# Kernel tuning notes

Measured on AMD Instinct MI355X. Metric: run time of the kernel, lower is better.

## Reference

```python
import jax, jax.numpy as jnp
import numpy as np

TEMPERATURE_F = 0.5  # init kwarg temperature_f
B = 4096
D = 256


def setup_inputs() -> dict:
    key = jax.random.key(0)
    k1, k2 = jax.random.split(key)
    h_i = jax.random.normal(k1, (B, D), dtype=jnp.float32)
    h_j = jax.random.normal(k2, (B, D), dtype=jnp.float32)
    return {"h_i": h_i, "h_j": h_j, "batch_size": B}


def reference(h_i, h_j, batch_size):
    # NT-Xent / InfoNCE (forward_feature_InfoNCE).
    # Original: logits = [pos | sim[neg_mask].reshape(N,-1)], labels = 0,
    # CrossEntropyLoss(reduction='sum') / N.
    # The logit set per row i is {positive} U {negatives} = all sim[i, :] except
    # the diagonal (self) entry, since neg_mask removes diagonal + positive pair
    # and the positive is prepended back. So CE reduces to logsumexp over the
    # off-diagonal row minus the positive logit.
    N = 2 * batch_size
    h = jnp.concatenate([h_i, h_j], axis=0)                    # [N, D]
    sim = jnp.matmul(h, h.T) / TEMPERATURE_F                   # [N, N]
    pos = jnp.concatenate([
        jnp.diagonal(sim, offset=batch_size),                  # sim_i_j
        jnp.diagonal(sim, offset=-batch_size),                 # sim_j_i
    ])                                                         # [N]
    denom_mask = ~jnp.eye(N, dtype=bool)                       # drop self-sim only
    neg_inf = jnp.finfo(sim.dtype).min
    lse = jax.nn.logsumexp(jnp.where(denom_mask, sim, neg_inf), axis=1)  # [N]
    loss = jnp.sum(lse - pos) / N
    return loss
```

## Files before the change

### kernel.cpp

```cpp
#include <hip/hip_runtime.h>
#include <stdint.h>

#define N_TOT 8192
#define DIM   256
#define BHALF 4096
#define BM    256
#define CT    64
#define NC    16
#define CW    (N_TOT / NC)
#define NTILE (CW / CT)

#define SCALEF 2.8853900817779268f
#define LN2F   0.69314718055994531f
#define SHIFT2 200.0f

typedef __attribute__((ext_vector_type(8))) short bf16x8;
typedef __attribute__((ext_vector_type(4))) float f32x4;

typedef const __attribute__((address_space(1))) void* gas_ptr;
typedef __attribute__((address_space(3))) void* lds_ptr;

#if __has_builtin(__builtin_amdgcn_exp2f)
__device__ inline float exp2v(float x) { return __builtin_amdgcn_exp2f(x); }
#else
__device__ inline float exp2v(float x) { return exp2f(x); }
#endif

__device__ inline float bf2f(ushort u) { return __uint_as_float(((uint32_t)u) << 16); }

__device__ inline ushort f2bf(float f) {
  uint32_t u = __float_as_uint(f);
  u = (u + 0x7fffu + ((u >> 16) & 1u)) >> 16;
  return (ushort)u;
}

__global__ void conv_kernel(const float* __restrict__ hi, const float* __restrict__ hj,
                            ushort* __restrict__ hb) {
  int t = blockIdx.x * blockDim.x + threadIdx.x;
  const int half4 = BHALF * DIM / 4;
  float4 v = (t < half4) ? ((const float4*)hi)[t] : ((const float4*)hj)[t - half4];
  ushort4 o;
  o.x = f2bf(v.x); o.y = f2bf(v.y); o.z = f2bf(v.z); o.w = f2bf(v.w);
  ((ushort4*)hb)[t] = o;
}

__global__ void pos_kernel(const ushort* __restrict__ hb, float* __restrict__ pos2) {
  int gw = (blockIdx.x * blockDim.x + threadIdx.x) >> 6;
  int l = threadIdx.x & 63;
  if (gw >= N_TOT) return;
  int j = (gw < BHALF) ? gw + BHALF : gw - BHALF;
  const ushort4* a = (const ushort4*)(hb + (size_t)gw * DIM);
  const ushort4* b = (const ushort4*)(hb + (size_t)j * DIM);
  ushort4 av = a[l], bv = b[l];
  float acc = bf2f(av.x) * bf2f(bv.x) + bf2f(av.y) * bf2f(bv.y)
            + bf2f(av.z) * bf2f(bv.z) + bf2f(av.w) * bf2f(bv.w);
  #pragma unroll
  for (int d = 1; d < 64; d <<= 1) acc += __shfl_xor(acc, d, 64);
  if (l == 0) pos2[gw] = acc * SCALEF;
}

__global__ __launch_bounds__(256, 1)
void lse_stage1(const ushort* __restrict__ hb, float* __restrict__ wsum) {
  const int tid = threadIdx.x;
  const int w  = tid >> 6;
  const int l  = tid & 63;
  const int lg = l >> 4;
  const int ll = l & 15;
  const int row0  = blockIdx.x * BM + w * 64;
  const int cbase = blockIdx.y * CW;

  __shared__ ushort Bt[2][CT * DIM];

  bf16x8 afrag[4][8];
  #pragma unroll
  for (int r = 0; r < 4; ++r) {
    const ushort* ap = hb + (size_t)(row0 + r * 16 + ll) * DIM + lg * 8;
    #pragma unroll
    for (int q = 0; q < 8; ++q) afrag[r][q] = *(const bf16x8*)(ap + q * 32);
  }

  float s[16];
  #pragma unroll
  for (int i = 0; i < 16; ++i) s[i] = 0.0f;
  const float NEGINF = -__builtin_inff();

  auto stage = [&](int buf, int t) {
    const int c0 = cbase + t * CT;
    #pragma unroll
    for (int q = 0; q < 8; ++q) {
      int a    = w * 8192 + q * 1024 + l * 16;
      int trow = a >> 9;
      int kb   = (a & 511) ^ ((trow & 7) << 4);
      const void* g = (const void*)((const char*)hb + ((size_t)(c0 + trow) * DIM) * 2 + kb);
      __builtin_amdgcn_global_load_lds((gas_ptr)g,
                                       (lds_ptr)((char*)&Bt[buf][0] + w * 8192 + q * 1024),
                                       16, 0, 0);
    }
  };

  stage(0, 0);
  asm volatile("s_waitcnt vmcnt(0)" ::: "memory");
  __syncthreads();

  for (int t = 0; t < NTILE; ++t) {
    const int cur = t & 1;
    const int c0  = cbase + t * CT;
    if (t + 1 < NTILE) stage(cur ^ 1, t + 1);

    const bool hasdiag = (c0 < row0 + 64) && (row0 < c0 + CT);

    for (int fg = 0; fg < 2; ++fg) {
      f32x4 acc[4][2];
      #pragma unroll
      for (int r = 0; r < 4; ++r)
        #pragma unroll
        for (int fi = 0; fi < 2; ++fi) acc[r][fi] = (f32x4){0.f, 0.f, 0.f, 0.f};

      #pragma unroll
      for (int q = 0; q < 8; ++q) {
        bf16x8 bfr[2];
        #pragma unroll
        for (int fi = 0; fi < 2; ++fi) {
          int brow = (fg * 2 + fi) * 16 + ll;
          int kb   = (q * 64 + lg * 16) ^ ((brow & 7) << 4);
          bfr[fi] = *(const bf16x8*)((const char*)&Bt[cur][0] + brow * 512 + kb);
        }
        #pragma unroll
        for (int r = 0; r < 4; ++r)
          #pragma unroll
          for (int fi = 0; fi < 2; ++fi)
            acc[r][fi] = __builtin_amdgcn_mfma_f32_16x16x32_bf16(afrag[r][q], bfr[fi],
                                                                 acc[r][fi], 0, 0, 0);
      }

      #pragma unroll
      for (int r = 0; r < 4; ++r) {
        #pragma unroll
        for (int j = 0; j < 4; ++j) {
          float v0 = acc[r][0][j], v1 = acc[r][1][j];
          if (hasdiag) {
            const int grow = row0 + r * 16 + lg * 4 + j;
            const int gc0  = c0 + ll + (fg * 2 + 0) * 16;
            const int gc1  = c0 + ll + (fg * 2 + 1) * 16;
            v0 = (grow == gc0) ? NEGINF : v0;
            v1 = (grow == gc1) ? NEGINF : v1;
          }
          float p0 = exp2v(__builtin_fmaf(v0, SCALEF, -SHIFT2));
          float p1 = exp2v(__builtin_fmaf(v1, SCALEF, -SHIFT2));
          s[r * 4 + j] += p0 + p1;
        }
      }
    }

    asm volatile("s_waitcnt vmcnt(0)" ::: "memory");
    __syncthreads();
  }

  #pragma unroll
  for (int i = 0; i < 16; ++i) {
    #pragma unroll
    for (int d = 1; d < 16; d <<= 1) s[i] += __shfl_xor(s[i], d, 16);
  }

  if (ll == 0) {
    #pragma unroll
    for (int r = 0; r < 4; ++r)
      #pragma unroll
      for (int j = 0; j < 4; ++j) {
        int grow = row0 + r * 16 + lg * 4 + j;
        wsum[blockIdx.y * N_TOT + grow] = s[r * 4 + j];
      }
  }
}

__global__ void finish_kernel(const float* __restrict__ wsum,
                              const float* __restrict__ pos2, float* __restrict__ partial) {
  const int i = blockIdx.x * blockDim.x + threadIdx.x;
  float S = 0.f;
  #pragma unroll
  for (int c = 0; c < NC; ++c) S += wsum[c * N_TOT + i];
  float lse2 = SHIFT2 + log2f(S);
  float contrib = (lse2 - pos2[i]) * (LN2F / (float)N_TOT);

  #pragma unroll
  for (int d = 32; d >= 1; d >>= 1) contrib += __shfl_down(contrib, d, 64);
  __shared__ float red[4];
  if ((threadIdx.x & 63) == 0) red[threadIdx.x >> 6] = contrib;
  __syncthreads();
  if (threadIdx.x == 0) partial[blockIdx.x] = red[0] + red[1] + red[2] + red[3];
}

__global__ void final_kernel(const float* __restrict__ partial, float* __restrict__ out) {
  int l = threadIdx.x;
  float v = (l < 32) ? partial[l] : 0.f;
  #pragma unroll
  for (int d = 32; d >= 1; d >>= 1) v += __shfl_down(v, d, 64);
  if (l == 0) out[0] = v;
}

extern "C" void kernel_launch(void* const* d_in, const int* in_sizes, int n_in,
                              void* d_out, int out_size, void* d_ws, size_t ws_size,
                              hipStream_t stream) {
  const float* hi = (const float*)d_in[0];
  const float* hj = (const float*)d_in[1];
  float* out = (float*)d_out;
  char* ws = (char*)d_ws;

  ushort* hb    = (ushort*)(ws);
  float*  wsum  = (float*)(ws + 4194304);
  float*  pos2  = (float*)(ws + 4194304 + 524288);
  float*  part  = (float*)(ws + 4194304 + 524288 + 32768);

  conv_kernel<<<N_TOT * DIM / 4 / 256, 256, 0, stream>>>(hi, hj, hb);
  pos_kernel<<<N_TOT / 4, 256, 0, stream>>>(hb, pos2);
  dim3 g1(N_TOT / BM, NC);
  lse_stage1<<<g1, 256, 0, stream>>>(hb, wsum);
  finish_kernel<<<N_TOT / 256, 256, 0, stream>>>(wsum, pos2, part);
  final_kernel<<<1, 64, 0, stream>>>(part, out);
}
```

Before: 61.09 us.

## Switch LSE GEMM to 32x32x16 MFMA tiles with wider LDS swizzle

Replaces the 16x16x32 bf16 MFMA tiling with 32x32x16 MFMA instructions, so each wave computes two 32-row blocks against 32-column B fragments and reuses each B fragment across both. This cuts the number of LDS B-fragment reads per MFMA and the instruction count per tile. The LDS XOR swizzle widens to 16 rows to match the new access pattern, and s_setprio is raised around the MFMA loop. Register pressure rises (32 row sums, 16-wide accumulators), and the epilogue row mapping and reductions are rewritten, which risks correctness and occupancy.

```diff
diff --git a/kernel.cpp b/kernel.cpp
--- a/kernel.cpp
+++ b/kernel.cpp
@@ -15,7 +15,7 @@
 #define SHIFT2 200.0f
 
 typedef __attribute__((ext_vector_type(8))) short bf16x8;
-typedef __attribute__((ext_vector_type(4))) float f32x4;
+typedef __attribute__((ext_vector_type(16))) float f32x16;
 
 typedef const __attribute__((address_space(1))) void* gas_ptr;
 typedef __attribute__((address_space(3))) void* lds_ptr;
@@ -64,24 +64,24 @@
   const int tid = threadIdx.x;
   const int w  = tid >> 6;
   const int l  = tid & 63;
-  const int lg = l >> 4;
-  const int ll = l & 15;
+  const int cl = l & 31;
+  const int hh = l >> 5;
   const int row0  = blockIdx.x * BM + w * 64;
   const int cbase = blockIdx.y * CW;
 
   __shared__ ushort Bt[2][CT * DIM];
 
-  bf16x8 afrag[4][8];
-  #pragma unroll
-  for (int r = 0; r < 4; ++r) {
-    const ushort* ap = hb + (size_t)(row0 + r * 16 + ll) * DIM + lg * 8;
-    #pragma unroll
-    for (int q = 0; q < 8; ++q) afrag[r][q] = *(const bf16x8*)(ap + q * 32);
-  }
-
-  float s[16];
-  #pragma unroll
-  for (int i = 0; i < 16; ++i) s[i] = 0.0f;
+  bf16x8 afrag[2][16];
+  #pragma unroll
+  for (int r = 0; r < 2; ++r) {
+    const ushort* ap = hb + (size_t)(row0 + r * 32 + cl) * DIM + hh * 8;
+    #pragma unroll
+    for (int q = 0; q < 16; ++q) afrag[r][q] = *(const bf16x8*)(ap + q * 16);
+  }
+
+  float s[32];
+  #pragma unroll
+  for (int i = 0; i < 32; ++i) s[i] = 0.0f;
   const float NEGINF = -__builtin_inff();
 
   auto stage = [&](int buf, int t) {
@@ -90,7 +90,7 @@
     for (int q = 0; q < 8; ++q) {
       int a    = w * 8192 + q * 1024 + l * 16;
       int trow = a >> 9;
-      int kb   = (a & 511) ^ ((trow & 7) << 4);
+      int kb   = (a & 511) ^ ((trow & 15) << 4);
       const void* g = (const void*)((const char*)hb + ((size_t)(c0 + trow) * DIM) * 2 + kb);
       __builtin_amdgcn_global_load_lds((gas_ptr)g,
                                        (lds_ptr)((char*)&Bt[buf][0] + w * 8192 + q * 1024),
@@ -109,46 +109,37 @@
 
     const bool hasdiag = (c0 < row0 + 64) && (row0 < c0 + CT);
 
-    for (int fg = 0; fg < 2; ++fg) {
-      f32x4 acc[4][2];
-      #pragma unroll
-      for (int r = 0; r < 4; ++r)
-        #pragma unroll
-        for (int fi = 0; fi < 2; ++fi) acc[r][fi] = (f32x4){0.f, 0.f, 0.f, 0.f};
-
-      #pragma unroll
-      for (int q = 0; q < 8; ++q) {
-        bf16x8 bfr[2];
-        #pragma unroll
-        for (int fi = 0; fi < 2; ++fi) {
-          int brow = (fg * 2 + fi) * 16 + ll;
-          int kb   = (q * 64 + lg * 16) ^ ((brow & 7) << 4);
-          bfr[fi] = *(const bf16x8*)((const char*)&Bt[cur][0] + brow * 512 + kb);
+    #pragma unroll
+    for (int f = 0; f < 2; ++f) {
+      f32x16 acc0 = {0.f}, acc1 = {0.f};
+      #pragma unroll
+      for (int e = 0; e < 16; ++e) { acc0[e] = 0.f; acc1[e] = 0.f; }
+
+      const int  brow  = f * 32 + cl;
+      const char* bbase = (const char*)&Bt[cur][0] + brow * 512;
+      const int  kxor  = (brow & 15) << 4;
+
+      __builtin_amdgcn_s_setprio(1);
+      #pragma unroll
+      for (int q = 0; q < 16; ++q) {
+        const int kb = (q * 32 + hh * 16) ^ kxor;
+        bf16x8 bfr = *(const bf16x8*)(bbase + kb);
+        acc0 = __builtin_amdgcn_mfma_f32_32x32x16_bf16(afrag[0][q], bfr, acc0, 0, 0, 0);
+        acc1 = __builtin_amdgcn_mfma_f32_32x32x16_bf16(afrag[1][q], bfr, acc1, 0, 0, 0);
+      }
+      __builtin_amdgcn_s_setprio(0);
+
+      const int gcol = c0 + f * 32 + cl;
+      #pragma unroll
+      for (int e = 0; e < 16; ++e) {
+        float v0 = acc0[e], v1 = acc1[e];
+        if (hasdiag) {
+          const int rr = (e & 3) + 8 * (e >> 2) + 4 * hh;
+          v0 = (row0 + rr      == gcol) ? NEGINF : v0;
+          v1 = (row0 + 32 + rr == gcol) ? NEGINF : v1;
         }
-        #pragma unroll
-        for (int r = 0; r < 4; ++r)
-          #pragma unroll
-          for (int fi = 0; fi < 2; ++fi)
-            acc[r][fi] = __builtin_amdgcn_mfma_f32_16x16x32_bf16(afrag[r][q], bfr[fi],
-                                                                 acc[r][fi], 0, 0, 0);
-      }
-
-      #pragma unroll
-      for (int r = 0; r < 4; ++r) {
-        #pragma unroll
-        for (int j = 0; j < 4; ++j) {
-          float v0 = acc[r][0][j], v1 = acc[r][1][j];
-          if (hasdiag) {
-            const int grow = row0 + r * 16 + lg * 4 + j;
-            const int gc0  = c0 + ll + (fg * 2 + 0) * 16;
-            const int gc1  = c0 + ll + (fg * 2 + 1) * 16;
-            v0 = (grow == gc0) ? NEGINF : v0;
-            v1 = (grow == gc1) ? NEGINF : v1;
-          }
-          float p0 = exp2v(__builtin_fmaf(v0, SCALEF, -SHIFT2));
-          float p1 = exp2v(__builtin_fmaf(v1, SCALEF, -SHIFT2));
-          s[r * 4 + j] += p0 + p1;
-        }
+        s[e]      += exp2v(__builtin_fmaf(v0, SCALEF, -SHIFT2));
+        s[16 + e] += exp2v(__builtin_fmaf(v1, SCALEF, -SHIFT2));
       }
     }
 
@@ -157,18 +148,18 @@
   }
 
   #pragma unroll
-  for (int i = 0; i < 16; ++i) {
-    #pragma unroll
-    for (int d = 1; d < 16; d <<= 1) s[i] += __shfl_xor(s[i], d, 16);
-  }
-
-  if (ll == 0) {
-    #pragma unroll
-    for (int r = 0; r < 4; ++r)
-      #pragma unroll
-      for (int j = 0; j < 4; ++j) {
-        int grow = row0 + r * 16 + lg * 4 + j;
-        wsum[blockIdx.y * N_TOT + grow] = s[r * 4 + j];
+  for (int i = 0; i < 32; ++i) {
+    #pragma unroll
+    for (int d = 1; d < 32; d <<= 1) s[i] += __shfl_xor(s[i], d, 64);
+  }
+
+  if (cl == 0) {
+    #pragma unroll
+    for (int r = 0; r < 2; ++r)
+      #pragma unroll
+      for (int e = 0; e < 16; ++e) {
+        int grow = row0 + r * 32 + (e & 3) + 8 * (e >> 2) + 4 * hh;
+        wsum[blockIdx.y * N_TOT + grow] = s[r * 16 + e];
       }
   }
 }
```

After: 66.59 us. 1.09x slower.
